# Optimization experiments

Hardware: AMD Instinct MI355X
Metric: run time of the kernel (lower is better)

The kernel has to match this reference:

```python
import jax, jax.numpy as jnp
import numpy as np

H = 128
N_ATOMS = 20000
N_BONDS = 60000
BATCH = 8


def _linear_params(key, fan_in, fan_out, bias=True):
    kw, kb = jax.random.split(key)
    lim = 1.0 / np.sqrt(fan_in)
    W = jax.random.uniform(kw, (fan_in, fan_out), jnp.float32, -lim, lim)
    if bias:
        b = jax.random.uniform(kb, (fan_out,), jnp.float32, -lim, lim)
        return W, b
    return W


def setup_inputs() -> dict:
    key = jax.random.key(0)
    ks = jax.random.split(key, 12)
    h = jax.random.normal(ks[0], (BATCH, N_ATOMS, H), jnp.float32)
    x = jax.random.normal(ks[1], (BATCH, N_ATOMS, 3), jnp.float32)
    bond_indices = jax.random.randint(ks[2], (N_BONDS, 2), 0, N_ATOMS, jnp.int64)
    Wm1, bm1 = _linear_params(ks[3], 2 * H + 1, H)
    Wm2, bm2 = _linear_params(ks[4], H, H)
    Wn1, bn1 = _linear_params(ks[5], 2 * H, H)
    Wn2, bn2 = _linear_params(ks[6], H, H)
    Wc1, bc1 = _linear_params(ks[7], H, H)
    # xavier_uniform gain=0.001 for final coord layer [1, H] in torch -> [H, 1] here
    lim = 0.001 * np.sqrt(6.0 / (H + 1))
    Wc2 = jax.random.uniform(ks[8], (H, 1), jnp.float32, -lim, lim)
    return dict(h=h, x=x, bond_indices=bond_indices,
                Wm1=Wm1, bm1=bm1, Wm2=Wm2, bm2=bm2,
                Wn1=Wn1, bn1=bn1, Wn2=Wn2, bn2=bn2,
                Wc1=Wc1, bc1=bc1, Wc2=Wc2)


def reference(h, x, bond_indices, Wm1, bm1, Wm2, bm2, Wn1, bn1, Wn2, bn2, Wc1, bc1, Wc2):
    silu = jax.nn.silu
    n_atoms = h.shape[1]
    src = bond_indices[:, 0]
    dst = bond_indices[:, 1]

    h_src = h[:, src, :]            # [B, E, H]
    h_dst = h[:, dst, :]
    coord_diff = x[:, dst, :] - x[:, src, :]   # [B, E, 3]
    dist = jnp.linalg.norm(coord_diff, axis=-1, keepdims=True)  # [B, E, 1]

    mi = jnp.concatenate([h_src, h_dst, dist], axis=-1)  # [B, E, 2H+1]
    messages = silu(silu(mi @ Wm1 + bm1) @ Wm2 + bm2)    # [B, E, H]

    aggregated = jnp.zeros_like(h).at[:, dst, :].add(messages).at[:, src, :].add(messages)

    h_in = jnp.concatenate([h, aggregated], axis=-1)     # [B, N, 2H]
    h_out = h + (silu(h_in @ Wn1 + bn1) @ Wn2 + bn2)

    coord_weights = silu(messages @ Wc1 + bc1) @ Wc2     # [B, E, 1]
    coord_diff_norm = coord_diff / (dist + 1e-8)
    upd = coord_diff_norm * coord_weights                # [B, E, 3]
    coord_update = jnp.zeros_like(x).at[:, dst, :].add(upd).at[:, src, :].add(-upd)

    ones = jnp.ones(src.shape[0], dtype=h.dtype)
    bond_counts = jnp.zeros(n_atoms, dtype=h.dtype).at[dst].add(ones).at[src].add(ones)
    bond_counts = jnp.clip(bond_counts, 1.0, None)
    x_out = x + coord_update / bond_counts[None, :, None]
    return h_out, x_out
```

## Files before the change

kernel.cpp:

```cpp
#include <hip/hip_runtime.h>


#define H      128
#define NA     20000
#define NB     60000
#define NBATCH 8
#define ADJ_CAP 32

typedef __bf16 bf16;
typedef __bf16 bf16x4 __attribute__((ext_vector_type(4)));
typedef __bf16 bf16x8 __attribute__((ext_vector_type(8)));
typedef float  f32x4  __attribute__((ext_vector_type(4)));

__device__ __forceinline__ float silu_f(float v) {
  float e = __expf(-v);
  return v * __builtin_amdgcn_rcpf(1.0f + e);
}

__device__ __forceinline__ int tswz(int row, int col) {
  return (row << 7) + (((((col) >> 3) ^ (row & 7)) << 3) | (col & 7));
}

__global__ void cast_h(const float* __restrict__ src, bf16* __restrict__ dst) {
  int i = blockIdx.x * 256 + threadIdx.x;
  float4 v = *(const float4*)(src + (size_t)i * 4);
  bf16x4 t = {(bf16)v.x, (bf16)v.y, (bf16)v.z, (bf16)v.w};
  *(bf16x4*)(dst + (size_t)i * 4) = t;
}

__global__ void pack_w(const float* __restrict__ src, bf16* __restrict__ dst,
                       int K) {
  int i = blockIdx.x * 256 + threadIdx.x;
  if (i >= K * 128) return;
  int k = i >> 7, n = i & 127;
  int nt = n >> 4, ks = k >> 5;
  int lane = (((k >> 3) & 3) << 4) | (n & 15);
  int j = k & 7;
  int KS = K >> 5;
  dst[((((nt * KS + ks) * 64) + lane) << 3) + j] = (bf16)src[i];
}

__global__ void build_adj2(const int* __restrict__ bonds,
                           int* __restrict__ degI, int* __restrict__ adj2) {
  int e = blockIdx.x * 256 + threadIdx.x;
  if (e >= NB) return;
  int s = bonds[2 * e], d = bonds[2 * e + 1];
  int p = atomicAdd(&degI[s], 1);
  if (p < ADJ_CAP) adj2[s * ADJ_CAP + p] = (e << 1);
  p = atomicAdd(&degI[d], 1);
  if (p < ADJ_CAP) adj2[d * ADJ_CAP + p] = (e << 1) | 1;
}

__global__ __launch_bounds__(256, 6) void msg_kernel(
    const bf16* __restrict__ hb, const float* __restrict__ x,
    const int* __restrict__ bonds,
    const bf16* __restrict__ W1p, const float* __restrict__ bm1,
    const bf16* __restrict__ W2p, const float* __restrict__ bm2,
    const float* __restrict__ w1c,
    const bf16* __restrict__ Wc1p, const float* __restrict__ bc1,
    const float* __restrict__ Wc2,
    bf16* __restrict__ msgOut, float* __restrict__ updv) {
  __shared__ __align__(16) bf16 Tbuf[32 * 128];
  __shared__ float cds[32 * 3];
  __shared__ float dists[32];
  __shared__ float bm1s[128], bm2s[128], w1cs[128], bc1s[128], wc2s[128];
  __shared__ float cwpart[2][32];

  const int tid = threadIdx.x, blk = blockIdx.x;

  if (tid < 32) {
    int Rg = blk * 32 + tid;
    int bond = Rg >> 3, batch = Rg & 7;
    int s = bonds[2 * bond], dn = bonds[2 * bond + 1];
    const float* xs = x + (size_t)(batch * NA + s) * 3;
    const float* xd = x + (size_t)(batch * NA + dn) * 3;
    float c0 = xd[0] - xs[0], c1 = xd[1] - xs[1], c2 = xd[2] - xs[2];
    cds[tid * 3 + 0] = c0; cds[tid * 3 + 1] = c1; cds[tid * 3 + 2] = c2;
    dists[tid] = sqrtf(c0 * c0 + c1 * c1 + c2 * c2);
  }
  if (tid < 128) {
    bm1s[tid] = bm1[tid]; bm2s[tid] = bm2[tid]; w1cs[tid] = w1c[tid];
    bc1s[tid] = bc1[tid]; wc2s[tid] = Wc2[tid];
  }
  __syncthreads();

  const int lane = tid & 63;
  const int quad = lane >> 4, l16 = lane & 15;
  const int wave = tid >> 6;
  const int rowBase = (wave >> 1) * 16;
  const int colG = wave & 1;
  const int colBase = colG * 64;
  const bf16x8* W1v = (const bf16x8*)W1p;
  const bf16x8* W2v = (const bf16x8*)W2p;
  const bf16x8* Wc1v = (const bf16x8*)Wc1p;

  const int RgA = blk * 32 + rowBase + l16;
  const int bondA = RgA >> 3, batA = RgA & 7;
  const bf16* hsrc = hb + (size_t)(batA * NA + bonds[2 * bondA]) * H;
  const bf16* hdst = hb + (size_t)(batA * NA + bonds[2 * bondA + 1]) * H;

  f32x4 acc[4];
#pragma unroll
  for (int nt = 0; nt < 4; nt++) acc[nt] = (f32x4){0.f, 0.f, 0.f, 0.f};

#pragma unroll
  for (int ks = 0; ks < 4; ks++) {
    bf16x8 a = *(const bf16x8*)(hsrc + ks * 32 + quad * 8);
#pragma unroll
    for (int nt = 0; nt < 4; nt++) {
      bf16x8 b = W1v[((colG * 4 + nt) * 8 + ks) * 64 + lane];
      acc[nt] = __builtin_amdgcn_mfma_f32_16x16x32_bf16(a, b, acc[nt], 0, 0, 0);
    }
  }
#pragma unroll
  for (int ks = 4; ks < 8; ks++) {
    bf16x8 a = *(const bf16x8*)(hdst + (ks - 4) * 32 + quad * 8);
#pragma unroll
    for (int nt = 0; nt < 4; nt++) {
      bf16x8 b = W1v[((colG * 4 + nt) * 8 + ks) * 64 + lane];
      acc[nt] = __builtin_amdgcn_mfma_f32_16x16x32_bf16(a, b, acc[nt], 0, 0, 0);
    }
  }
#pragma unroll
  for (int nt = 0; nt < 4; nt++) {
    int col = colBase + nt * 16 + l16;
    float bb = bm1s[col], wc = w1cs[col];
#pragma unroll
    for (int reg = 0; reg < 4; reg++) {
      int row = rowBase + quad * 4 + reg;
      float v = acc[nt][reg] + bb + dists[row] * wc;
      Tbuf[tswz(row, col)] = (bf16)silu_f(v);
    }
  }
  __syncthreads();

#pragma unroll
  for (int nt = 0; nt < 4; nt++) acc[nt] = (f32x4){0.f, 0.f, 0.f, 0.f};
#pragma unroll
  for (int ks = 0; ks < 4; ks++) {
    bf16x8 a = *(const bf16x8*)&Tbuf[tswz(rowBase + l16, ks * 32 + quad * 8)];
#pragma unroll
    for (int nt = 0; nt < 4; nt++) {
      bf16x8 b = W2v[((colG * 4 + nt) * 4 + ks) * 64 + lane];
      acc[nt] = __builtin_amdgcn_mfma_f32_16x16x32_bf16(a, b, acc[nt], 0, 0, 0);
    }
  }
  __syncthreads();
#pragma unroll
  for (int nt = 0; nt < 4; nt++) {
    int col = colBase + nt * 16 + l16;
    float bb = bm2s[col];
#pragma unroll
    for (int reg = 0; reg < 4; reg++) {
      int row = rowBase + quad * 4 + reg;
      Tbuf[tswz(row, col)] = (bf16)silu_f(acc[nt][reg] + bb);
    }
  }
  __syncthreads();

#pragma unroll
  for (int nt = 0; nt < 4; nt++) acc[nt] = (f32x4){0.f, 0.f, 0.f, 0.f};
#pragma unroll
  for (int ks = 0; ks < 4; ks++) {
    bf16x8 a = *(const bf16x8*)&Tbuf[tswz(rowBase + l16, ks * 32 + quad * 8)];
#pragma unroll
    for (int nt = 0; nt < 4; nt++) {
      bf16x8 b = Wc1v[((colG * 4 + nt) * 4 + ks) * 64 + lane];
      acc[nt] = __builtin_amdgcn_mfma_f32_16x16x32_bf16(a, b, acc[nt], 0, 0, 0);
    }
  }

#pragma unroll
  for (int i = 0; i < 2; i++) {
    int item = i * 64 + lane;
    int row = rowBase + (item >> 3);
    int cg = colG * 8 + (item & 7);
    *(bf16x8*)&msgOut[(size_t)(blk * 32 + row) * H + cg * 8] =
        *(const bf16x8*)&Tbuf[tswz(row, cg * 8)];
  }

  float cwp[4] = {0.f, 0.f, 0.f, 0.f};
#pragma unroll
  for (int nt = 0; nt < 4; nt++) {
    int col = colBase + nt * 16 + l16;
    float bb = bc1s[col], w2 = wc2s[col];
#pragma unroll
    for (int reg = 0; reg < 4; reg++)
      cwp[reg] += silu_f(acc[nt][reg] + bb) * w2;
  }
#pragma unroll
  for (int reg = 0; reg < 4; reg++) {
    float s = cwp[reg];
    s += __shfl_xor(s, 1);
    s += __shfl_xor(s, 2);
    s += __shfl_xor(s, 4);
    s += __shfl_xor(s, 8);
    cwp[reg] = s;
  }
  if (l16 == 0) {
#pragma unroll
    for (int reg = 0; reg < 4; reg++)
      cwpart[colG][rowBase + quad * 4 + reg] = cwp[reg];
  }
  __syncthreads();
  if (colG == 0 && l16 == 0) {
#pragma unroll
    for (int reg = 0; reg < 4; reg++) {
      int row = rowBase + quad * 4 + reg;
      size_t Rg = (size_t)blk * 32 + row;
      float cw = cwpart[0][row] + cwpart[1][row];
      float inv = 1.0f / (dists[row] + 1e-8f);
#pragma unroll
      for (int c = 0; c < 3; c++)
        updv[Rg * 3 + c] = cds[row * 3 + c] * inv * cw;
    }
  }
}

__global__ __launch_bounds__(256, 6) void node_kernel(
    const float* __restrict__ h, const bf16* __restrict__ hb,
    const bf16* __restrict__ msg, const float* __restrict__ updv,
    const int* __restrict__ degI, const int* __restrict__ adj2,
    const bf16* __restrict__ Wn1p, const float* __restrict__ bn1,
    const bf16* __restrict__ Wn2p, const float* __restrict__ bn2,
    const float* __restrict__ x,
    float* __restrict__ hout, float* __restrict__ xout) {
  __shared__ __align__(16) bf16 Abuf[32 * 128];
  __shared__ __align__(16) bf16 Tbuf[32 * 128];

  const int tid = threadIdx.x, blk = blockIdx.x;

  {
    const int row = tid >> 3, c8 = tid & 7;
    const int Rg = blk * 32 + row;
    const int atomA = Rg % NA, batA = Rg / NA;
    int deg = degI[atomA];
    if (deg > ADJ_CAP) deg = ADJ_CAP;
    const int* ap = adj2 + atomA * ADJ_CAP;
    float a16[16];
#pragma unroll
    for (int t = 0; t < 16; t++) a16[t] = 0.f;
    float sx = 0.f, sy = 0.f, sz = 0.f;
    int j = 0;
    for (; j + 2 <= deg; j += 2) {
      int ent0 = ap[j], ent1 = ap[j + 1];
      const bf16* m0 = msg + ((size_t)(ent0 >> 1) * 8 + batA) * H + c8 * 16;
      const bf16* m1 = msg + ((size_t)(ent1 >> 1) * 8 + batA) * H + c8 * 16;
      bf16x8 v0 = *(const bf16x8*)(m0);
      bf16x8 v1 = *(const bf16x8*)(m0 + 8);
      bf16x8 u0 = *(const bf16x8*)(m1);
      bf16x8 u1 = *(const bf16x8*)(m1 + 8);
      if (c8 == 0) {
        float sg0 = (ent0 & 1) ? 1.0f : -1.0f;
        float sg1 = (ent1 & 1) ? 1.0f : -1.0f;
        const float* uv0 = updv + ((size_t)(ent0 >> 1) * 8 + batA) * 3;
        const float* uv1 = updv + ((size_t)(ent1 >> 1) * 8 + batA) * 3;
        sx += sg0 * uv0[0] + sg1 * uv1[0];
        sy += sg0 * uv0[1] + sg1 * uv1[1];
        sz += sg0 * uv0[2] + sg1 * uv1[2];
      }
#pragma unroll
      for (int t = 0; t < 8; t++) {
        a16[t]     += (float)v0[t] + (float)u0[t];
        a16[8 + t] += (float)v1[t] + (float)u1[t];
      }
    }
    if (j < deg) {
      int ent0 = ap[j];
      const bf16* m0 = msg + ((size_t)(ent0 >> 1) * 8 + batA) * H + c8 * 16;
      bf16x8 v0 = *(const bf16x8*)(m0);
      bf16x8 v1 = *(const bf16x8*)(m0 + 8);
      if (c8 == 0) {
        float sg0 = (ent0 & 1) ? 1.0f : -1.0f;
        const float* uv0 = updv + ((size_t)(ent0 >> 1) * 8 + batA) * 3;
        sx += sg0 * uv0[0]; sy += sg0 * uv0[1]; sz += sg0 * uv0[2];
      }
#pragma unroll
      for (int t = 0; t < 8; t++) {
        a16[t]     += (float)v0[t];
        a16[8 + t] += (float)v1[t];
      }
    }
    if (c8 == 0) {
      float cnt = deg < 1 ? 1.0f : (float)deg;
      float inv = 1.0f / cnt;
      size_t o = (size_t)Rg * 3;
      xout[o + 0] = x[o + 0] + sx * inv;
      xout[o + 1] = x[o + 1] + sy * inv;
      xout[o + 2] = x[o + 2] + sz * inv;
    }
    bf16x8 w0, w1;
#pragma unroll
    for (int t = 0; t < 8; t++) { w0[t] = (bf16)a16[t]; w1[t] = (bf16)a16[8 + t]; }
    *(bf16x8*)&Abuf[tswz(row, c8 * 16)]     = w0;
    *(bf16x8*)&Abuf[tswz(row, c8 * 16 + 8)] = w1;
  }
  __syncthreads();

  const int lane = tid & 63, wave = tid >> 6;
  const int quad = lane >> 4, l16 = lane & 15;
  const int rowG = (wave >> 1) * 16, colG = wave & 1, colBase = colG * 64;
  const int RgA = blk * 32 + rowG + l16;
  const bf16* hrow = hb + (size_t)RgA * H;
  const bf16x8* W1v = (const bf16x8*)Wn1p;
  const bf16x8* W2v = (const bf16x8*)Wn2p;

  f32x4 acc[4];
#pragma unroll
  for (int nt = 0; nt < 4; nt++) acc[nt] = (f32x4){0.f, 0.f, 0.f, 0.f};

#pragma unroll
  for (int ks = 0; ks < 4; ks++) {
    bf16x8 a = *(const bf16x8*)(hrow + ks * 32 + quad * 8);
#pragma unroll
    for (int nt = 0; nt < 4; nt++) {
      bf16x8 b = W1v[((colG * 4 + nt) * 8 + ks) * 64 + lane];
      acc[nt] = __builtin_amdgcn_mfma_f32_16x16x32_bf16(a, b, acc[nt], 0, 0, 0);
    }
  }
#pragma unroll
  for (int ks2 = 0; ks2 < 4; ks2++) {
    bf16x8 a = *(const bf16x8*)&Abuf[tswz(rowG + l16, ks2 * 32 + quad * 8)];
#pragma unroll
    for (int nt = 0; nt < 4; nt++) {
      bf16x8 b = W1v[((colG * 4 + nt) * 8 + 4 + ks2) * 64 + lane];
      acc[nt] = __builtin_amdgcn_mfma_f32_16x16x32_bf16(a, b, acc[nt], 0, 0, 0);
    }
  }
#pragma unroll
  for (int nt = 0; nt < 4; nt++) {
    int col = colBase + nt * 16 + l16;
    float bb = bn1[col];
#pragma unroll
    for (int reg = 0; reg < 4; reg++) {
      int row = rowG + quad * 4 + reg;
      Tbuf[tswz(row, col)] = (bf16)silu_f(acc[nt][reg] + bb);
    }
  }
  __syncthreads();

#pragma unroll
  for (int nt = 0; nt < 4; nt++) acc[nt] = (f32x4){0.f, 0.f, 0.f, 0.f};
#pragma unroll
  for (int ks = 0; ks < 4; ks++) {
    bf16x8 a = *(const bf16x8*)&Tbuf[tswz(rowG + l16, ks * 32 + quad * 8)];
#pragma unroll
    for (int nt = 0; nt < 4; nt++) {
      bf16x8 b = W2v[((colG * 4 + nt) * 4 + ks) * 64 + lane];
      acc[nt] = __builtin_amdgcn_mfma_f32_16x16x32_bf16(a, b, acc[nt], 0, 0, 0);
    }
  }
#pragma unroll
  for (int nt = 0; nt < 4; nt++) {
    int col = colBase + nt * 16 + l16;
    float bb = bn2[col];
#pragma unroll
    for (int reg = 0; reg < 4; reg++) {
      size_t Ro = (size_t)blk * 32 + rowG + quad * 4 + reg;
      hout[Ro * H + col] = h[Ro * H + col] + acc[nt][reg] + bb;
    }
  }
}

extern "C" void kernel_launch(void* const* d_in, const int* in_sizes, int n_in,
                              void* d_out, int out_size, void* d_ws,
                              size_t ws_size, hipStream_t stream) {
  const float* h    = (const float*)d_in[0];
  const float* x    = (const float*)d_in[1];
  const int*  bonds = (const int*)d_in[2];
  const float* Wm1  = (const float*)d_in[3];
  const float* bm1  = (const float*)d_in[4];
  const float* Wm2  = (const float*)d_in[5];
  const float* bm2  = (const float*)d_in[6];
  const float* Wn1  = (const float*)d_in[7];
  const float* bn1  = (const float*)d_in[8];
  const float* Wn2  = (const float*)d_in[9];
  const float* bn2  = (const float*)d_in[10];
  const float* Wc1  = (const float*)d_in[11];
  const float* bc1  = (const float*)d_in[12];
  const float* Wc2  = (const float*)d_in[13];

  float* out  = (float*)d_out;
  float* hout = out;
  float* xout = out + (size_t)NBATCH * NA * H;

  char* ws = (char*)d_ws;
  const size_t OFF_DEG  = 0;
  const size_t OFF_W1   = 163840;
  const size_t OFF_W2   = OFF_W1 + 65536;
  const size_t OFF_WN1  = OFF_W2 + 32768;
  const size_t OFF_WN2  = OFF_WN1 + 65536;
  const size_t OFF_WC1  = OFF_WN2 + 32768;
  const size_t OFF_ADJ2 = 393216;
  const size_t OFF_UPDV = 2953216;
  const size_t OFF_HB   = 8713216;
  const size_t OFF_MSG  = 49673216;

  int*   degI = (int*)(ws + OFF_DEG);
  bf16*  W1p  = (bf16*)(ws + OFF_W1);
  bf16*  W2p  = (bf16*)(ws + OFF_W2);
  bf16*  Wn1p = (bf16*)(ws + OFF_WN1);
  bf16*  Wn2p = (bf16*)(ws + OFF_WN2);
  bf16*  Wc1p = (bf16*)(ws + OFF_WC1);
  int*   adj2 = (int*)(ws + OFF_ADJ2);
  float* updv = (float*)(ws + OFF_UPDV);
  bf16*  hb   = (bf16*)(ws + OFF_HB);
  bf16*  msgB = (bf16*)(ws + OFF_MSG);

  (void)hipMemsetAsync(degI, 0, NA * sizeof(int), stream);

  cast_h<<<NBATCH * NA * H / 1024, 256, 0, stream>>>(h, hb);
  pack_w<<<128, 256, 0, stream>>>(Wm1, W1p, 256);
  pack_w<<<64, 256, 0, stream>>>(Wm2, W2p, 128);
  pack_w<<<128, 256, 0, stream>>>(Wn1, Wn1p, 256);
  pack_w<<<64, 256, 0, stream>>>(Wn2, Wn2p, 128);
  pack_w<<<64, 256, 0, stream>>>(Wc1, Wc1p, 128);

  build_adj2<<<(NB + 255) / 256, 256, 0, stream>>>(bonds, degI, adj2);

  msg_kernel<<<NB * NBATCH / 32, 256, 0, stream>>>(
      hb, x, bonds, W1p, bm1, W2p, bm2, Wm1 + 256 * H, Wc1p, bc1, Wc2,
      msgB, updv);
  node_kernel<<<NBATCH * NA / 32, 256, 0, stream>>>(
      h, hb, msgB, updv, degI, adj2, Wn1p, bn1, Wn2p, bn2, x,
      hout, xout);
}
```

Before: 508.2 us.

## Make msg_kernel persistent with register-resident weight fragments

Turns msg_kernel into a persistent kernel of 512 blocks of 512 threads, each looping over 16-row edge tiles. Each of the 8 waves owns a 16-column slice and keeps its W1/W2/Wc1 MFMA fragments and bias values in registers for the whole run, so weights are no longer re-fetched per tile. Coordinate differences and distances for the next tile are double-buffered in shared memory. In exchange, tiles shrink to 16 rows with several block-wide barriers per tile, and the large register footprint may limit occupancy and latency hiding for the gathered h loads.

```diff
diff --git a/kernel.cpp b/kernel.cpp
--- a/kernel.cpp
+++ b/kernel.cpp
@@ -6,6 +6,8 @@
 #define NB     60000
 #define NBATCH 8
 #define ADJ_CAP 32
+#define NT_TILES (NB * NBATCH / 16)
+#define MSG_GRID 512
 
 typedef __bf16 bf16;
 typedef __bf16 bf16x4 __attribute__((ext_vector_type(4)));
@@ -51,7 +53,7 @@
   if (p < ADJ_CAP) adj2[d * ADJ_CAP + p] = (e << 1) | 1;
 }
 
-__global__ __launch_bounds__(256, 6) void msg_kernel(
+__global__ __launch_bounds__(512, 4) void msg_kernel(
     const bf16* __restrict__ hb, const float* __restrict__ x,
     const int* __restrict__ bonds,
     const bf16* __restrict__ W1p, const float* __restrict__ bm1,
@@ -60,160 +62,139 @@
     const bf16* __restrict__ Wc1p, const float* __restrict__ bc1,
     const float* __restrict__ Wc2,
     bf16* __restrict__ msgOut, float* __restrict__ updv) {
-  __shared__ __align__(16) bf16 Tbuf[32 * 128];
-  __shared__ float cds[32 * 3];
-  __shared__ float dists[32];
-  __shared__ float bm1s[128], bm2s[128], w1cs[128], bc1s[128], wc2s[128];
-  __shared__ float cwpart[2][32];
-
-  const int tid = threadIdx.x, blk = blockIdx.x;
-
-  if (tid < 32) {
-    int Rg = blk * 32 + tid;
-    int bond = Rg >> 3, batch = Rg & 7;
+  __shared__ __align__(16) bf16 T[16 * 128];
+  __shared__ float cds[2][16 * 3];
+  __shared__ float dists[2][16];
+  __shared__ float cwpart[8][16];
+
+  const int tid = threadIdx.x;
+  const int lane = tid & 63, w = tid >> 6;
+  const int quad = lane >> 4, l16 = lane & 15;
+  const int colW = w * 16 + l16;
+
+  const bf16x8* W1v  = (const bf16x8*)W1p;
+  const bf16x8* W2v  = (const bf16x8*)W2p;
+  const bf16x8* Wc1v = (const bf16x8*)Wc1p;
+  bf16x8 w1f[8], w2f[4], wc1f[4];
+#pragma unroll
+  for (int ks = 0; ks < 8; ks++) w1f[ks] = W1v[(w * 8 + ks) * 64 + lane];
+#pragma unroll
+  for (int ks = 0; ks < 4; ks++) w2f[ks] = W2v[(w * 4 + ks) * 64 + lane];
+#pragma unroll
+  for (int ks = 0; ks < 4; ks++) wc1f[ks] = Wc1v[(w * 4 + ks) * 64 + lane];
+  const float bm1c = bm1[colW], w1cc = w1c[colW], bm2c = bm2[colW];
+  const float bc1c = bc1[colW], wc2c = Wc2[colW];
+
+  int buf = 0;
+  if (tid < 16) {
+    int Rg = blockIdx.x * 16 + tid;
+    int bond = Rg >> 3, bt = Rg & 7;
     int s = bonds[2 * bond], dn = bonds[2 * bond + 1];
-    const float* xs = x + (size_t)(batch * NA + s) * 3;
-    const float* xd = x + (size_t)(batch * NA + dn) * 3;
+    const float* xs = x + (size_t)(bt * NA + s) * 3;
+    const float* xd = x + (size_t)(bt * NA + dn) * 3;
     float c0 = xd[0] - xs[0], c1 = xd[1] - xs[1], c2 = xd[2] - xs[2];
-    cds[tid * 3 + 0] = c0; cds[tid * 3 + 1] = c1; cds[tid * 3 + 2] = c2;
-    dists[tid] = sqrtf(c0 * c0 + c1 * c1 + c2 * c2);
-  }
-  if (tid < 128) {
-    bm1s[tid] = bm1[tid]; bm2s[tid] = bm2[tid]; w1cs[tid] = w1c[tid];
-    bc1s[tid] = bc1[tid]; wc2s[tid] = Wc2[tid];
+    cds[0][tid * 3 + 0] = c0; cds[0][tid * 3 + 1] = c1;
+    cds[0][tid * 3 + 2] = c2;
+    dists[0][tid] = sqrtf(c0 * c0 + c1 * c1 + c2 * c2);
   }
   __syncthreads();
 
-  const int lane = tid & 63;
-  const int quad = lane >> 4, l16 = lane & 15;
-  const int wave = tid >> 6;
-  const int rowBase = (wave >> 1) * 16;
-  const int colG = wave & 1;
-  const int colBase = colG * 64;
-  const bf16x8* W1v = (const bf16x8*)W1p;
-  const bf16x8* W2v = (const bf16x8*)W2p;
-  const bf16x8* Wc1v = (const bf16x8*)Wc1p;
-
-  const int RgA = blk * 32 + rowBase + l16;
-  const int bondA = RgA >> 3, batA = RgA & 7;
-  const bf16* hsrc = hb + (size_t)(batA * NA + bonds[2 * bondA]) * H;
-  const bf16* hdst = hb + (size_t)(batA * NA + bonds[2 * bondA + 1]) * H;
-
-  f32x4 acc[4];
-#pragma unroll
-  for (int nt = 0; nt < 4; nt++) acc[nt] = (f32x4){0.f, 0.f, 0.f, 0.f};
-
-#pragma unroll
-  for (int ks = 0; ks < 4; ks++) {
-    bf16x8 a = *(const bf16x8*)(hsrc + ks * 32 + quad * 8);
-#pragma unroll
-    for (int nt = 0; nt < 4; nt++) {
-      bf16x8 b = W1v[((colG * 4 + nt) * 8 + ks) * 64 + lane];
-      acc[nt] = __builtin_amdgcn_mfma_f32_16x16x32_bf16(a, b, acc[nt], 0, 0, 0);
-    }
-  }
-#pragma unroll
-  for (int ks = 4; ks < 8; ks++) {
-    bf16x8 a = *(const bf16x8*)(hdst + (ks - 4) * 32 + quad * 8);
-#pragma unroll
-    for (int nt = 0; nt < 4; nt++) {
-      bf16x8 b = W1v[((colG * 4 + nt) * 8 + ks) * 64 + lane];
-      acc[nt] = __builtin_amdgcn_mfma_f32_16x16x32_bf16(a, b, acc[nt], 0, 0, 0);
-    }
-  }
-#pragma unroll
-  for (int nt = 0; nt < 4; nt++) {
-    int col = colBase + nt * 16 + l16;
-    float bb = bm1s[col], wc = w1cs[col];
+  for (int t = blockIdx.x; t < NT_TILES; t += MSG_GRID) {
+    const int Rg = t * 16 + l16;
+    const int bond = Rg >> 3, bat = Rg & 7;
+    const int sA = bonds[2 * bond], dA = bonds[2 * bond + 1];
+    const bf16* hs = hb + (size_t)(bat * NA + sA) * H;
+    const bf16* hd = hb + (size_t)(bat * NA + dA) * H;
+    bf16x8 a[8];
+#pragma unroll
+    for (int ks = 0; ks < 4; ks++)
+      a[ks] = *(const bf16x8*)(hs + ks * 32 + quad * 8);
+#pragma unroll
+    for (int ks = 0; ks < 4; ks++)
+      a[4 + ks] = *(const bf16x8*)(hd + ks * 32 + quad * 8);
+
+    f32x4 acc = (f32x4){0.f, 0.f, 0.f, 0.f};
+#pragma unroll
+    for (int ks = 0; ks < 8; ks++)
+      acc = __builtin_amdgcn_mfma_f32_16x16x32_bf16(a[ks], w1f[ks], acc, 0, 0, 0);
 #pragma unroll
     for (int reg = 0; reg < 4; reg++) {
-      int row = rowBase + quad * 4 + reg;
-      float v = acc[nt][reg] + bb + dists[row] * wc;
-      Tbuf[tswz(row, col)] = (bf16)silu_f(v);
-    }
-  }
-  __syncthreads();
-
-#pragma unroll
-  for (int nt = 0; nt < 4; nt++) acc[nt] = (f32x4){0.f, 0.f, 0.f, 0.f};
-#pragma unroll
-  for (int ks = 0; ks < 4; ks++) {
-    bf16x8 a = *(const bf16x8*)&Tbuf[tswz(rowBase + l16, ks * 32 + quad * 8)];
-#pragma unroll
-    for (int nt = 0; nt < 4; nt++) {
-      bf16x8 b = W2v[((colG * 4 + nt) * 4 + ks) * 64 + lane];
-      acc[nt] = __builtin_amdgcn_mfma_f32_16x16x32_bf16(a, b, acc[nt], 0, 0, 0);
-    }
-  }
-  __syncthreads();
-#pragma unroll
-  for (int nt = 0; nt < 4; nt++) {
-    int col = colBase + nt * 16 + l16;
-    float bb = bm2s[col];
+      int row = quad * 4 + reg;
+      float v = acc[reg] + bm1c + dists[buf][row] * w1cc;
+      T[tswz(row, colW)] = (bf16)silu_f(v);
+    }
+    __syncthreads();
+
+    f32x4 acc2 = (f32x4){0.f, 0.f, 0.f, 0.f};
+#pragma unroll
+    for (int ks = 0; ks < 4; ks++) {
+      bf16x8 aa = *(const bf16x8*)&T[tswz(l16, ks * 32 + quad * 8)];
+      acc2 = __builtin_amdgcn_mfma_f32_16x16x32_bf16(aa, w2f[ks], acc2, 0, 0, 0);
+    }
+    if (tid < 16) {
+      int tn = t + MSG_GRID;
+      if (tn < NT_TILES) {
+        int Rg2 = tn * 16 + tid;
+        int bond2 = Rg2 >> 3, bt2 = Rg2 & 7;
+        int s2 = bonds[2 * bond2], dn2 = bonds[2 * bond2 + 1];
+        const float* xs = x + (size_t)(bt2 * NA + s2) * 3;
+        const float* xd = x + (size_t)(bt2 * NA + dn2) * 3;
+        float c0 = xd[0] - xs[0], c1 = xd[1] - xs[1], c2 = xd[2] - xs[2];
+        cds[buf ^ 1][tid * 3 + 0] = c0; cds[buf ^ 1][tid * 3 + 1] = c1;
+        cds[buf ^ 1][tid * 3 + 2] = c2;
+        dists[buf ^ 1][tid] = sqrtf(c0 * c0 + c1 * c1 + c2 * c2);
+      }
+    }
+    __syncthreads();
 #pragma unroll
     for (int reg = 0; reg < 4; reg++) {
-      int row = rowBase + quad * 4 + reg;
-      Tbuf[tswz(row, col)] = (bf16)silu_f(acc[nt][reg] + bb);
-    }
-  }
-  __syncthreads();
-
-#pragma unroll
-  for (int nt = 0; nt < 4; nt++) acc[nt] = (f32x4){0.f, 0.f, 0.f, 0.f};
-#pragma unroll
-  for (int ks = 0; ks < 4; ks++) {
-    bf16x8 a = *(const bf16x8*)&Tbuf[tswz(rowBase + l16, ks * 32 + quad * 8)];
-#pragma unroll
-    for (int nt = 0; nt < 4; nt++) {
-      bf16x8 b = Wc1v[((colG * 4 + nt) * 4 + ks) * 64 + lane];
-      acc[nt] = __builtin_amdgcn_mfma_f32_16x16x32_bf16(a, b, acc[nt], 0, 0, 0);
-    }
-  }
-
-#pragma unroll
-  for (int i = 0; i < 2; i++) {
-    int item = i * 64 + lane;
-    int row = rowBase + (item >> 3);
-    int cg = colG * 8 + (item & 7);
-    *(bf16x8*)&msgOut[(size_t)(blk * 32 + row) * H + cg * 8] =
-        *(const bf16x8*)&Tbuf[tswz(row, cg * 8)];
-  }
-
-  float cwp[4] = {0.f, 0.f, 0.f, 0.f};
-#pragma unroll
-  for (int nt = 0; nt < 4; nt++) {
-    int col = colBase + nt * 16 + l16;
-    float bb = bc1s[col], w2 = wc2s[col];
+      int row = quad * 4 + reg;
+      T[tswz(row, colW)] = (bf16)silu_f(acc2[reg] + bm2c);
+    }
+    __syncthreads();
+
+    if (tid < 256) {
+      int row = tid >> 4, cg = tid & 15;
+      *(bf16x8*)&msgOut[(size_t)(t * 16 + row) * H + cg * 8] =
+          *(const bf16x8*)&T[tswz(row, cg * 8)];
+    }
+    f32x4 acc3 = (f32x4){0.f, 0.f, 0.f, 0.f};
+#pragma unroll
+    for (int ks = 0; ks < 4; ks++) {
+      bf16x8 aa = *(const bf16x8*)&T[tswz(l16, ks * 32 + quad * 8)];
+      acc3 = __builtin_amdgcn_mfma_f32_16x16x32_bf16(aa, wc1f[ks], acc3, 0, 0, 0);
+    }
+    float cwp[4];
 #pragma unroll
     for (int reg = 0; reg < 4; reg++)
-      cwp[reg] += silu_f(acc[nt][reg] + bb) * w2;
-  }
-#pragma unroll
-  for (int reg = 0; reg < 4; reg++) {
-    float s = cwp[reg];
-    s += __shfl_xor(s, 1);
-    s += __shfl_xor(s, 2);
-    s += __shfl_xor(s, 4);
-    s += __shfl_xor(s, 8);
-    cwp[reg] = s;
-  }
-  if (l16 == 0) {
-#pragma unroll
-    for (int reg = 0; reg < 4; reg++)
-      cwpart[colG][rowBase + quad * 4 + reg] = cwp[reg];
-  }
-  __syncthreads();
-  if (colG == 0 && l16 == 0) {
+      cwp[reg] = silu_f(acc3[reg] + bc1c) * wc2c;
 #pragma unroll
     for (int reg = 0; reg < 4; reg++) {
-      int row = rowBase + quad * 4 + reg;
-      size_t Rg = (size_t)blk * 32 + row;
-      float cw = cwpart[0][row] + cwpart[1][row];
-      float inv = 1.0f / (dists[row] + 1e-8f);
+      float s = cwp[reg];
+      s += __shfl_xor(s, 1);
+      s += __shfl_xor(s, 2);
+      s += __shfl_xor(s, 4);
+      s += __shfl_xor(s, 8);
+      cwp[reg] = s;
+    }
+    if (l16 == 0) {
+#pragma unroll
+      for (int reg = 0; reg < 4; reg++)
+        cwpart[w][quad * 4 + reg] = cwp[reg];
+    }
+    __syncthreads();
+
+    if (tid < 16) {
+      float cw = 0.f;
+#pragma unroll
+      for (int ww = 0; ww < 8; ww++) cw += cwpart[ww][tid];
+      float inv = 1.0f / (dists[buf][tid] + 1e-8f);
+      size_t R = (size_t)t * 16 + tid;
 #pragma unroll
       for (int c = 0; c < 3; c++)
-        updv[Rg * 3 + c] = cds[row * 3 + c] * inv * cw;
-    }
+        updv[R * 3 + c] = cds[buf][tid * 3 + c] * inv * cw;
+    }
+    buf ^= 1;
   }
 }
 
@@ -418,7 +399,7 @@
 
   build_adj2<<<(NB + 255) / 256, 256, 0, stream>>>(bonds, degI, adj2);
 
-  msg_kernel<<<NB * NBATCH / 32, 256, 0, stream>>>(
+  msg_kernel<<<MSG_GRID, 512, 0, stream>>>(
       hb, x, bonds, W1p, bm1, W2p, bm2, Wm1 + 256 * H, Wc1p, bc1, Wc2,
       msgB, updv);
   node_kernel<<<NBATCH * NA / 32, 256, 0, stream>>>(
```

Measured after the change: 609.5 us. 19.9% more time.
